# Performance work log

Hardware: AMD Instinct MI355X
Metric: run time of the kernel (lower is better)

The kernel has to match this reference:

```python
import jax, jax.numpy as jnp
import numpy as np

N_NODES = 50000
N_EDGES = 600000
F_IN = 128
HID = 128
N_CLASSES = 10


def _gcn_graph(edge_index, n_nodes):
    # PyG GCNConv: add self-loops, deg computed on target (col) with weight 1,
    # norm_e = deg^-1/2[src] * deg^-1/2[dst]
    src = jnp.concatenate([edge_index[0], jnp.arange(n_nodes, dtype=edge_index.dtype)])
    dst = jnp.concatenate([edge_index[1], jnp.arange(n_nodes, dtype=edge_index.dtype)])
    deg = jax.ops.segment_sum(jnp.ones_like(dst, dtype=jnp.float32), dst, num_segments=n_nodes)
    dinv = jnp.where(deg > 0, jax.lax.rsqrt(deg), 0.0)
    norm = dinv[src] * dinv[dst]  # [E+N]
    return src, dst, norm


def _gcn_layer(x, W, b, src, dst, norm, n_nodes):
    h = x @ W                      # [N, out] linear first (bias applied post-agg)
    m = h[src] * norm[:, None]     # gather + scale, [E+N, out]
    out = jax.ops.segment_sum(m, dst, num_segments=n_nodes)  # scatter-add
    return out + b


def setup_inputs() -> dict:
    key = jax.random.key(0)
    ks = jax.random.split(key, 4)
    x = jax.random.normal(ks[0], (N_NODES, F_IN), dtype=jnp.float32)
    edge_index = jax.random.randint(ks[1], (2, N_EDGES), 0, N_NODES, dtype=jnp.int64)
    # Glorot-ish init scale for weights
    W_stack = jax.random.normal(ks[2], (8, HID, HID), dtype=jnp.float32) * (1.0 / np.sqrt(HID))
    b_stack = jnp.zeros((8, HID), dtype=jnp.float32)
    W_out = jax.random.normal(ks[3], (HID, N_CLASSES), dtype=jnp.float32) * (1.0 / np.sqrt(HID))
    b_out = jnp.zeros((N_CLASSES,), dtype=jnp.float32)
    return {"x": x, "edge_index": edge_index, "W_stack": W_stack, "b_stack": b_stack,
            "W_out": W_out, "b_out": b_out}


def reference(x, edge_index, W_stack, b_stack, W_out, b_out):
    n_nodes = x.shape[0]
    src, dst, norm = _gcn_graph(edge_index, n_nodes)
    h = x
    for i in range(8):  # conv1..conv8 with ELU
        h = jax.nn.elu(_gcn_layer(h, W_stack[i], b_stack[i], src, dst, norm, n_nodes))
    # conv9: no activation
    return _gcn_layer(h, W_out, b_out, src, dst, norm, n_nodes)
```

## Files before the change

kernel.cpp:

```cpp
#include <hip/hip_runtime.h>
#include <math.h>

#define NN 50000
#define NE 600000
#define HID 128
#define NCLS 10
#define BK 32


__global__ __launch_bounds__(256) void k_count(const int* __restrict__ edge,
                                               int* __restrict__ counts) {
    int e = blockIdx.x * 256 + threadIdx.x;
    if (e < NE) atomicAdd(&counts[edge[NE + e]], 1);
}

__device__ __forceinline__ int wave_incl_scan(int x, int lane) {
#pragma unroll
    for (int off = 1; off < 64; off <<= 1) {
        int y = __shfl_up(x, off, 64);
        if (lane >= off) x += y;
    }
    return x;
}

__global__ __launch_bounds__(256) void k_scan1(const int* __restrict__ counts,
                                               int* __restrict__ rowptr,
                                               int* __restrict__ bsum,
                                               float* __restrict__ dinv) {
    __shared__ int ws[4];
    int tid = threadIdx.x;
    int i = blockIdx.x * 256 + tid;
    int lane = tid & 63, wv = tid >> 6;
    int v = (i < NN) ? counts[i] : 0;
    if (i < NN) dinv[i] = rsqrtf((float)(v + 1));
    int x = wave_incl_scan(v, lane);
    if (lane == 63) ws[wv] = x;
    __syncthreads();
    int off = 0;
    for (int j = 0; j < wv; ++j) off += ws[j];
    if (i < NN) rowptr[i] = off + x - v;
    if (tid == 255) bsum[blockIdx.x] = off + x;
}

__global__ __launch_bounds__(256) void k_scan2(int* __restrict__ bsum, int n) {
    __shared__ int ws[4];
    int tid = threadIdx.x;
    int lane = tid & 63, wv = tid >> 6;
    int v = (tid < n) ? bsum[tid] : 0;
    int x = wave_incl_scan(v, lane);
    if (lane == 63) ws[wv] = x;
    __syncthreads();
    int off = 0;
    for (int j = 0; j < wv; ++j) off += ws[j];
    __syncthreads();
    if (tid < n) bsum[tid] = off + x - v;
}

__global__ __launch_bounds__(256) void k_scan3(int* __restrict__ rowptr,
                                               const int* __restrict__ bsum) {
    int i = blockIdx.x * 256 + threadIdx.x;
    if (i < NN) rowptr[i] += bsum[blockIdx.x];
    if (i == 0) rowptr[NN] = NE;
}

__global__ __launch_bounds__(256) void k_fill(const int* __restrict__ edge,
                                              const int* __restrict__ rowptr,
                                              int* __restrict__ cursor,
                                              const float* __restrict__ dinv,
                                              int2* __restrict__ csr) {
    int e = blockIdx.x * 256 + threadIdx.x;
    if (e >= NE) return;
    int s = edge[e], d = edge[NE + e];
    int p = rowptr[d] + atomicAdd(&cursor[d], 1);
    csr[p] = make_int2(s, __float_as_int(dinv[s] * dinv[d]));
}


__global__ __launch_bounds__(256) void k_matmul128(const float* __restrict__ H,
                                                   const float* __restrict__ W,
                                                   float* __restrict__ T) {
    __shared__ float As[BK * 128];
    __shared__ float Bs[BK * 128];
    int tid = threadIdx.x;
    int lane = tid & 63, w = tid >> 6;
    int wr = lane >> 3, wc = lane & 7;
    int wy = w >> 1, wx = w & 1;
    int lr0 = wy * 64 + wr * 8;
    int lc0 = wx * 64 + wc * 8;
    int rowBase = blockIdx.x * 128;

    int sa_row = tid >> 1;
    int sa_k = (tid & 1) * 16;
    int sa_grow = rowBase + sa_row;
    if (sa_grow >= NN) sa_grow = NN - 1;

    float acc[8][8];
#pragma unroll
    for (int i = 0; i < 8; ++i)
#pragma unroll
        for (int j = 0; j < 8; ++j) acc[i][j] = 0.f;

    for (int k0 = 0; k0 < HID; k0 += BK) {
        const float4* hsrc = (const float4*)(H + (size_t)sa_grow * HID + k0 + sa_k);
        float4 a0 = hsrc[0], a1 = hsrc[1], a2 = hsrc[2], a3 = hsrc[3];
        const float4* wsrc = (const float4*)(W + (size_t)k0 * HID);
        float4 b0 = wsrc[tid], b1 = wsrc[tid + 256], b2 = wsrc[tid + 512], b3 = wsrc[tid + 768];
        __syncthreads();
        As[(sa_k + 0) * 128 + sa_row] = a0.x;  As[(sa_k + 1) * 128 + sa_row] = a0.y;
        As[(sa_k + 2) * 128 + sa_row] = a0.z;  As[(sa_k + 3) * 128 + sa_row] = a0.w;
        As[(sa_k + 4) * 128 + sa_row] = a1.x;  As[(sa_k + 5) * 128 + sa_row] = a1.y;
        As[(sa_k + 6) * 128 + sa_row] = a1.z;  As[(sa_k + 7) * 128 + sa_row] = a1.w;
        As[(sa_k + 8) * 128 + sa_row] = a2.x;  As[(sa_k + 9) * 128 + sa_row] = a2.y;
        As[(sa_k + 10) * 128 + sa_row] = a2.z; As[(sa_k + 11) * 128 + sa_row] = a2.w;
        As[(sa_k + 12) * 128 + sa_row] = a3.x; As[(sa_k + 13) * 128 + sa_row] = a3.y;
        As[(sa_k + 14) * 128 + sa_row] = a3.z; As[(sa_k + 15) * 128 + sa_row] = a3.w;
        ((float4*)Bs)[tid] = b0;
        ((float4*)Bs)[tid + 256] = b1;
        ((float4*)Bs)[tid + 512] = b2;
        ((float4*)Bs)[tid + 768] = b3;
        __syncthreads();
#pragma unroll
        for (int kk = 0; kk < BK; ++kk) {
            float a[8], b[8];
            ((float4*)a)[0] = *(const float4*)&As[kk * 128 + lr0];
            ((float4*)a)[1] = *(const float4*)&As[kk * 128 + lr0 + 4];
            ((float4*)b)[0] = *(const float4*)&Bs[kk * 128 + lc0];
            ((float4*)b)[1] = *(const float4*)&Bs[kk * 128 + lc0 + 4];
#pragma unroll
            for (int i = 0; i < 8; ++i)
#pragma unroll
                for (int j = 0; j < 8; ++j) acc[i][j] += a[i] * b[j];
        }
    }
#pragma unroll
    for (int i = 0; i < 8; ++i) {
        int gr = rowBase + lr0 + i;
        if (gr < NN) {
            float4 o0 = {acc[i][0], acc[i][1], acc[i][2], acc[i][3]};
            float4 o1 = {acc[i][4], acc[i][5], acc[i][6], acc[i][7]};
            float4* dst = (float4*)(T + (size_t)gr * HID + lc0);
            dst[0] = o0;
            dst[1] = o1;
        }
    }
}


__global__ __launch_bounds__(256) void k_gather_agg(const float* __restrict__ T,
                                                    float* __restrict__ Hout,
                                                    const int* __restrict__ rowptr,
                                                    const int2* __restrict__ csr,
                                                    const float* __restrict__ dinv,
                                                    const float* __restrict__ bias) {
    int lane = threadIdx.x & 63;
    int node = (blockIdx.x * 256 + threadIdx.x) >> 6;
    if (node >= NN) return;
    int slot = lane >> 4, c16 = lane & 15;

    int beg = rowptr[node], end = rowptr[node + 1];
    float4 acc0 = {0.f, 0.f, 0.f, 0.f}, acc1 = {0.f, 0.f, 0.f, 0.f};
    const int2 zed = make_int2(0, 0);

    int i = beg + slot;
    int2 e0 = (i < end) ? csr[i] : zed;
    int2 e1 = (i + 4 < end) ? csr[i + 4] : zed;
    for (; i < end; i += 8) {
        int2 p0 = (i + 8 < end) ? csr[i + 8] : zed;
        int2 p1 = (i + 12 < end) ? csr[i + 12] : zed;
        const float4* s0 = (const float4*)(T + (size_t)e0.x * HID) + c16 * 2;
        const float4* s1 = (const float4*)(T + (size_t)e1.x * HID) + c16 * 2;
        float4 u0 = s0[0], u1 = s0[1];
        float4 v0 = s1[0], v1 = s1[1];
        float w0 = __int_as_float(e0.y);
        float w1 = __int_as_float(e1.y);
        acc0.x += w0 * u0.x; acc0.y += w0 * u0.y; acc0.z += w0 * u0.z; acc0.w += w0 * u0.w;
        acc1.x += w0 * u1.x; acc1.y += w0 * u1.y; acc1.z += w0 * u1.z; acc1.w += w0 * u1.w;
        acc0.x += w1 * v0.x; acc0.y += w1 * v0.y; acc0.z += w1 * v0.z; acc0.w += w1 * v0.w;
        acc1.x += w1 * v1.x; acc1.y += w1 * v1.y; acc1.z += w1 * v1.z; acc1.w += w1 * v1.w;
        e0 = p0; e1 = p1;
    }
    acc0.x += __shfl_xor(acc0.x, 16, 64); acc0.y += __shfl_xor(acc0.y, 16, 64);
    acc0.z += __shfl_xor(acc0.z, 16, 64); acc0.w += __shfl_xor(acc0.w, 16, 64);
    acc1.x += __shfl_xor(acc1.x, 16, 64); acc1.y += __shfl_xor(acc1.y, 16, 64);
    acc1.z += __shfl_xor(acc1.z, 16, 64); acc1.w += __shfl_xor(acc1.w, 16, 64);
    acc0.x += __shfl_xor(acc0.x, 32, 64); acc0.y += __shfl_xor(acc0.y, 32, 64);
    acc0.z += __shfl_xor(acc0.z, 32, 64); acc0.w += __shfl_xor(acc0.w, 32, 64);
    acc1.x += __shfl_xor(acc1.x, 32, 64); acc1.y += __shfl_xor(acc1.y, 32, 64);
    acc1.z += __shfl_xor(acc1.z, 32, 64); acc1.w += __shfl_xor(acc1.w, 32, 64);

    if (slot == 0) {
        float sn = dinv[node];
        sn *= sn;
        const float4* trow = (const float4*)(T + (size_t)node * HID) + c16 * 2;
        float4 t0 = trow[0], t1 = trow[1];
        const float4* b4 = (const float4*)bias + c16 * 2;
        float4 b0 = b4[0], b1 = b4[1];
        float4 r0, r1;
        r0.x = acc0.x + sn * t0.x + b0.x; r0.y = acc0.y + sn * t0.y + b0.y;
        r0.z = acc0.z + sn * t0.z + b0.z; r0.w = acc0.w + sn * t0.w + b0.w;
        r1.x = acc1.x + sn * t1.x + b1.x; r1.y = acc1.y + sn * t1.y + b1.y;
        r1.z = acc1.z + sn * t1.z + b1.z; r1.w = acc1.w + sn * t1.w + b1.w;
        r0.x = r0.x > 0.f ? r0.x : expm1f(r0.x);
        r0.y = r0.y > 0.f ? r0.y : expm1f(r0.y);
        r0.z = r0.z > 0.f ? r0.z : expm1f(r0.z);
        r0.w = r0.w > 0.f ? r0.w : expm1f(r0.w);
        r1.x = r1.x > 0.f ? r1.x : expm1f(r1.x);
        r1.y = r1.y > 0.f ? r1.y : expm1f(r1.y);
        r1.z = r1.z > 0.f ? r1.z : expm1f(r1.z);
        r1.w = r1.w > 0.f ? r1.w : expm1f(r1.w);
        float4* dst = (float4*)(Hout + (size_t)node * HID) + c16 * 2;
        dst[0] = r0;
        dst[1] = r1;
    }
}


__global__ __launch_bounds__(256) void k_matmul_out(const float* __restrict__ H,
                                                    const float* __restrict__ W,
                                                    float* __restrict__ T2) {
    __shared__ float Ws[128 * 11];
    int tid = threadIdx.x;
    for (int m = tid; m < HID * NCLS; m += 256) {
        int k = m / NCLS, c = m - k * NCLS;
        Ws[k * 11 + c] = W[m];
    }
    __syncthreads();
    int row = (blockIdx.x * 256 + tid) >> 4;
    int c16 = tid & 15;
    if (row >= NN) return;
    const float* h = H + (size_t)row * HID;
    float acc[NCLS];
#pragma unroll
    for (int c = 0; c < NCLS; ++c) acc[c] = 0.f;
#pragma unroll
    for (int j = 0; j < 8; ++j) {
        float hv = h[c16 + 16 * j];
        const float* wr = &Ws[(c16 + 16 * j) * 11];
#pragma unroll
        for (int c = 0; c < NCLS; ++c) acc[c] += hv * wr[c];
    }
#pragma unroll
    for (int off = 8; off >= 1; off >>= 1) {
#pragma unroll
        for (int c = 0; c < NCLS; ++c) acc[c] += __shfl_xor(acc[c], off, 16);
    }
    if (c16 < NCLS) T2[(size_t)row * NCLS + c16] = acc[c16];
}

__global__ __launch_bounds__(256) void k_gather_out(const float* __restrict__ T2,
                                                    float* __restrict__ out,
                                                    const int* __restrict__ rowptr,
                                                    const int2* __restrict__ csr,
                                                    const float* __restrict__ dinv,
                                                    const float* __restrict__ bias) {
    int lane = threadIdx.x & 63;
    int node = (blockIdx.x * 256 + threadIdx.x) >> 6;
    if (node >= NN) return;
    int slot = lane >> 4, c = lane & 15;
    int beg = rowptr[node], end = rowptr[node + 1];
    float acc = 0.f;
    if (c < NCLS) {
        for (int i = beg + slot; i < end; i += 4) {
            int2 e = csr[i];
            acc += __int_as_float(e.y) * T2[(size_t)e.x * NCLS + c];
        }
    }
    acc += __shfl_xor(acc, 16, 64);
    acc += __shfl_xor(acc, 32, 64);
    if (slot == 0 && c < NCLS) {
        float sn = dinv[node];
        sn *= sn;
        out[node * NCLS + c] = acc + sn * T2[(size_t)node * NCLS + c] + bias[c];
    }
}


extern "C" void kernel_launch(void* const* d_in, const int* in_sizes, int n_in,
                              void* d_out, int out_size, void* d_ws, size_t ws_size,
                              hipStream_t stream) {
    (void)in_sizes; (void)n_in; (void)out_size; (void)ws_size;
    const float* x       = (const float*)d_in[0];
    const int*   edge    = (const int*)d_in[1];
    const float* W_stack = (const float*)d_in[2];
    const float* b_stack = (const float*)d_in[3];
    const float* W_out   = (const float*)d_in[4];
    const float* b_out   = (const float*)d_in[5];
    float* out = (float*)d_out;

    char* ws = (char*)d_ws;
    const size_t bigbuf = (size_t)NN * HID * sizeof(float);
    float* X      = (float*)ws;
    float* Y      = (float*)(ws + bigbuf);
    char*  p      = ws + 2 * bigbuf;
    int2*  csr    = (int2*)p;              p += sizeof(int2) * NE;
    float* dinv   = (float*)p;             p += sizeof(float) * NN;
    int*   rowptr = (int*)p;               p += sizeof(int) * (NN + 1);
    int*   counts = (int*)p;               p += sizeof(int) * NN;
    int*   bsum   = (int*)p;               p += sizeof(int) * 256;

    const int NB_N  = (NN + 255) / 256;
    const int NB_E  = (NE + 255) / 256;
    const int NB_MM = (NN + 127) / 128;
    const int NB_W  = (NN * 64 + 255) / 256;
    const int NB_O  = (NN * 16 + 255) / 256;

    hipMemsetAsync(counts, 0, sizeof(int) * NN, stream);
    k_count<<<NB_E, 256, 0, stream>>>(edge, counts);
    k_scan1<<<NB_N, 256, 0, stream>>>(counts, rowptr, bsum, dinv);
    k_scan2<<<1, 256, 0, stream>>>(bsum, NB_N);
    k_scan3<<<NB_N, 256, 0, stream>>>(rowptr, bsum);
    hipMemsetAsync(counts, 0, sizeof(int) * NN, stream);
    k_fill<<<NB_E, 256, 0, stream>>>(edge, rowptr, counts, dinv, csr);

    const float* Hin = x;
    for (int l = 0; l < 8; ++l) {
        k_matmul128<<<NB_MM, 256, 0, stream>>>(Hin, W_stack + (size_t)l * HID * HID, Y);
        k_gather_agg<<<NB_W, 256, 0, stream>>>(Y, X, rowptr, csr, dinv,
                                               b_stack + (size_t)l * HID);
        Hin = X;
    }

    k_matmul_out<<<NB_O, 256, 0, stream>>>(X, W_out, Y);
    k_gather_out<<<NB_W, 256, 0, stream>>>(Y, out, rowptr, csr, dinv, b_out);
}
```

Before: 810.1 us.

## Double-buffer matmul shared tiles and coalesce gather-agg row loads

The 128-wide matmul now uses BK=16 with two shared-memory buffers, prefetching the next K-slice into registers while computing the current one and needing only one barrier per step. Separately, the gather-aggregate kernel changes each lane's float4 access pattern from two adjacent float4s to float4s at c16 and c16+16, so the 16 lanes read contiguous 256-byte halves of a row. This is meant to hide global load latency in the GEMM and coalesce the gather. The cost is more loop iterations and more registers held for the prefetched data.

```diff
diff --git a/kernel.cpp b/kernel.cpp
--- a/kernel.cpp
+++ b/kernel.cpp
@@ -5,7 +5,7 @@
 #define NE 600000
 #define HID 128
 #define NCLS 10
-#define BK 32
+#define BK 16
 
 
 __global__ __launch_bounds__(256) void k_count(const int* __restrict__ edge,
@@ -79,8 +79,8 @@
 __global__ __launch_bounds__(256) void k_matmul128(const float* __restrict__ H,
                                                    const float* __restrict__ W,
                                                    float* __restrict__ T) {
-    __shared__ float As[BK * 128];
-    __shared__ float Bs[BK * 128];
+    __shared__ float As[2][BK * 128];
+    __shared__ float Bs[2][BK * 128];
     int tid = threadIdx.x;
     int lane = tid & 63, w = tid >> 6;
     int wr = lane >> 3, wc = lane & 7;
@@ -90,9 +90,10 @@
     int rowBase = blockIdx.x * 128;
 
     int sa_row = tid >> 1;
-    int sa_k = (tid & 1) * 16;
+    int sa_k = (tid & 1) * 8;
     int sa_grow = rowBase + sa_row;
     if (sa_grow >= NN) sa_grow = NN - 1;
+    const float* hbase = H + (size_t)sa_grow * HID + sa_k;
 
     float acc[8][8];
 #pragma unroll
@@ -100,36 +101,49 @@
 #pragma unroll
         for (int j = 0; j < 8; ++j) acc[i][j] = 0.f;
 
-    for (int k0 = 0; k0 < HID; k0 += BK) {
-        const float4* hsrc = (const float4*)(H + (size_t)sa_grow * HID + k0 + sa_k);
-        float4 a0 = hsrc[0], a1 = hsrc[1], a2 = hsrc[2], a3 = hsrc[3];
-        const float4* wsrc = (const float4*)(W + (size_t)k0 * HID);
-        float4 b0 = wsrc[tid], b1 = wsrc[tid + 256], b2 = wsrc[tid + 512], b3 = wsrc[tid + 768];
-        __syncthreads();
-        As[(sa_k + 0) * 128 + sa_row] = a0.x;  As[(sa_k + 1) * 128 + sa_row] = a0.y;
-        As[(sa_k + 2) * 128 + sa_row] = a0.z;  As[(sa_k + 3) * 128 + sa_row] = a0.w;
-        As[(sa_k + 4) * 128 + sa_row] = a1.x;  As[(sa_k + 5) * 128 + sa_row] = a1.y;
-        As[(sa_k + 6) * 128 + sa_row] = a1.z;  As[(sa_k + 7) * 128 + sa_row] = a1.w;
-        As[(sa_k + 8) * 128 + sa_row] = a2.x;  As[(sa_k + 9) * 128 + sa_row] = a2.y;
-        As[(sa_k + 10) * 128 + sa_row] = a2.z; As[(sa_k + 11) * 128 + sa_row] = a2.w;
-        As[(sa_k + 12) * 128 + sa_row] = a3.x; As[(sa_k + 13) * 128 + sa_row] = a3.y;
-        As[(sa_k + 14) * 128 + sa_row] = a3.z; As[(sa_k + 15) * 128 + sa_row] = a3.w;
-        ((float4*)Bs)[tid] = b0;
-        ((float4*)Bs)[tid + 256] = b1;
-        ((float4*)Bs)[tid + 512] = b2;
-        ((float4*)Bs)[tid + 768] = b3;
+    {
+        float4 a0 = ((const float4*)hbase)[0];
+        float4 a1 = ((const float4*)hbase)[1];
+        const float4* wsrc = (const float4*)W;
+        float4 b0 = wsrc[tid], b1 = wsrc[tid + 256];
+        As[0][(sa_k + 0) * 128 + sa_row] = a0.x; As[0][(sa_k + 1) * 128 + sa_row] = a0.y;
+        As[0][(sa_k + 2) * 128 + sa_row] = a0.z; As[0][(sa_k + 3) * 128 + sa_row] = a0.w;
+        As[0][(sa_k + 4) * 128 + sa_row] = a1.x; As[0][(sa_k + 5) * 128 + sa_row] = a1.y;
+        As[0][(sa_k + 6) * 128 + sa_row] = a1.z; As[0][(sa_k + 7) * 128 + sa_row] = a1.w;
+        ((float4*)Bs[0])[tid] = b0;
+        ((float4*)Bs[0])[tid + 256] = b1;
+    }
+
+    for (int t = 0; t < 8; ++t) {
+        int cur = t & 1;
+        float4 na0, na1, nb0, nb1;
+        if (t < 7) {
+            const float4* hn = (const float4*)(hbase + (t + 1) * BK);
+            na0 = hn[0]; na1 = hn[1];
+            const float4* wn = (const float4*)(W + (size_t)(t + 1) * BK * HID);
+            nb0 = wn[tid]; nb1 = wn[tid + 256];
+        }
         __syncthreads();
 #pragma unroll
         for (int kk = 0; kk < BK; ++kk) {
             float a[8], b[8];
-            ((float4*)a)[0] = *(const float4*)&As[kk * 128 + lr0];
-            ((float4*)a)[1] = *(const float4*)&As[kk * 128 + lr0 + 4];
-            ((float4*)b)[0] = *(const float4*)&Bs[kk * 128 + lc0];
-            ((float4*)b)[1] = *(const float4*)&Bs[kk * 128 + lc0 + 4];
+            ((float4*)a)[0] = *(const float4*)&As[cur][kk * 128 + lr0];
+            ((float4*)a)[1] = *(const float4*)&As[cur][kk * 128 + lr0 + 4];
+            ((float4*)b)[0] = *(const float4*)&Bs[cur][kk * 128 + lc0];
+            ((float4*)b)[1] = *(const float4*)&Bs[cur][kk * 128 + lc0 + 4];
 #pragma unroll
             for (int i = 0; i < 8; ++i)
 #pragma unroll
                 for (int j = 0; j < 8; ++j) acc[i][j] += a[i] * b[j];
+        }
+        if (t < 7) {
+            int nxt = 1 - cur;
+            As[nxt][(sa_k + 0) * 128 + sa_row] = na0.x; As[nxt][(sa_k + 1) * 128 + sa_row] = na0.y;
+            As[nxt][(sa_k + 2) * 128 + sa_row] = na0.z; As[nxt][(sa_k + 3) * 128 + sa_row] = na0.w;
+            As[nxt][(sa_k + 4) * 128 + sa_row] = na1.x; As[nxt][(sa_k + 5) * 128 + sa_row] = na1.y;
+            As[nxt][(sa_k + 6) * 128 + sa_row] = na1.z; As[nxt][(sa_k + 7) * 128 + sa_row] = na1.w;
+            ((float4*)Bs[nxt])[tid] = nb0;
+            ((float4*)Bs[nxt])[tid + 256] = nb1;
         }
     }
 #pragma unroll
@@ -167,10 +181,10 @@
     for (; i < end; i += 8) {
         int2 p0 = (i + 8 < end) ? csr[i + 8] : zed;
         int2 p1 = (i + 12 < end) ? csr[i + 12] : zed;
-        const float4* s0 = (const float4*)(T + (size_t)e0.x * HID) + c16 * 2;
-        const float4* s1 = (const float4*)(T + (size_t)e1.x * HID) + c16 * 2;
-        float4 u0 = s0[0], u1 = s0[1];
-        float4 v0 = s1[0], v1 = s1[1];
+        const float4* s0 = (const float4*)(T + (size_t)e0.x * HID);
+        const float4* s1 = (const float4*)(T + (size_t)e1.x * HID);
+        float4 u0 = s0[c16], u1 = s0[c16 + 16];
+        float4 v0 = s1[c16], v1 = s1[c16 + 16];
         float w0 = __int_as_float(e0.y);
         float w1 = __int_as_float(e1.y);
         acc0.x += w0 * u0.x; acc0.y += w0 * u0.y; acc0.z += w0 * u0.z; acc0.w += w0 * u0.w;
@@ -191,10 +205,10 @@
     if (slot == 0) {
         float sn = dinv[node];
         sn *= sn;
-        const float4* trow = (const float4*)(T + (size_t)node * HID) + c16 * 2;
-        float4 t0 = trow[0], t1 = trow[1];
-        const float4* b4 = (const float4*)bias + c16 * 2;
-        float4 b0 = b4[0], b1 = b4[1];
+        const float4* trow = (const float4*)(T + (size_t)node * HID);
+        float4 t0 = trow[c16], t1 = trow[c16 + 16];
+        const float4* b4 = (const float4*)bias;
+        float4 b0 = b4[c16], b1 = b4[c16 + 16];
         float4 r0, r1;
         r0.x = acc0.x + sn * t0.x + b0.x; r0.y = acc0.y + sn * t0.y + b0.y;
         r0.z = acc0.z + sn * t0.z + b0.z; r0.w = acc0.w + sn * t0.w + b0.w;
@@ -208,9 +222,9 @@
         r1.y = r1.y > 0.f ? r1.y : expm1f(r1.y);
         r1.z = r1.z > 0.f ? r1.z : expm1f(r1.z);
         r1.w = r1.w > 0.f ? r1.w : expm1f(r1.w);
-        float4* dst = (float4*)(Hout + (size_t)node * HID) + c16 * 2;
-        dst[0] = r0;
-        dst[1] = r1;
+        float4* dst = (float4*)(Hout + (size_t)node * HID);
+        dst[c16] = r0;
+        dst[c16 + 16] = r1;
     }
 }
 
```

New measurement: 912.6 us. 1.13x slower.

## Fuse whole GCN pipeline into one cooperative persistent kernel with grid syncs

Applied to the files above, without the earlier changes.

Replaces the sequence of roughly 25 kernel launches with a single cooperative persistent kernel that runs CSR construction, all matmul and gather layers, and the output layer as phases separated by grid-wide syncs. It also overlaps the first-layer matmul with the graph-building phase and changes the gather lane mapping so the 16 lanes in a slot read contiguous float4 elements. The aim is to remove per-launch overhead and idle gaps between small kernels. In exchange, grid syncs cost time, persistent blocks loop over fixed tiles with possible load imbalance, and launch_bounds(256,4) may limit registers for the 8x8 matmul accumulators.

```diff
diff --git a/kernel.cpp b/kernel.cpp
--- a/kernel.cpp
+++ b/kernel.cpp
@@ -1,18 +1,19 @@
 #include <hip/hip_runtime.h>
+#include <hip/hip_cooperative_groups.h>
 #include <math.h>
+
+namespace cg = cooperative_groups;
 
 #define NN 50000
 #define NE 600000
 #define HID 128
 #define NCLS 10
-#define BK 32
-
-
-__global__ __launch_bounds__(256) void k_count(const int* __restrict__ edge,
-                                               int* __restrict__ counts) {
-    int e = blockIdx.x * 256 + threadIdx.x;
-    if (e < NE) atomicAdd(&counts[edge[NE + e]], 1);
-}
+#define MMBK 32
+#define NTILE 391
+#define NCHUNK 196
+#define NGRP4 12500
+#define NGRP16 3125
+
 
 __device__ __forceinline__ int wave_incl_scan(int x, int lane) {
 #pragma unroll
@@ -23,71 +24,16 @@
     return x;
 }
 
-__global__ __launch_bounds__(256) void k_scan1(const int* __restrict__ counts,
-                                               int* __restrict__ rowptr,
-                                               int* __restrict__ bsum,
-                                               float* __restrict__ dinv) {
-    __shared__ int ws[4];
-    int tid = threadIdx.x;
-    int i = blockIdx.x * 256 + tid;
-    int lane = tid & 63, wv = tid >> 6;
-    int v = (i < NN) ? counts[i] : 0;
-    if (i < NN) dinv[i] = rsqrtf((float)(v + 1));
-    int x = wave_incl_scan(v, lane);
-    if (lane == 63) ws[wv] = x;
-    __syncthreads();
-    int off = 0;
-    for (int j = 0; j < wv; ++j) off += ws[j];
-    if (i < NN) rowptr[i] = off + x - v;
-    if (tid == 255) bsum[blockIdx.x] = off + x;
-}
-
-__global__ __launch_bounds__(256) void k_scan2(int* __restrict__ bsum, int n) {
-    __shared__ int ws[4];
-    int tid = threadIdx.x;
-    int lane = tid & 63, wv = tid >> 6;
-    int v = (tid < n) ? bsum[tid] : 0;
-    int x = wave_incl_scan(v, lane);
-    if (lane == 63) ws[wv] = x;
-    __syncthreads();
-    int off = 0;
-    for (int j = 0; j < wv; ++j) off += ws[j];
-    __syncthreads();
-    if (tid < n) bsum[tid] = off + x - v;
-}
-
-__global__ __launch_bounds__(256) void k_scan3(int* __restrict__ rowptr,
-                                               const int* __restrict__ bsum) {
-    int i = blockIdx.x * 256 + threadIdx.x;
-    if (i < NN) rowptr[i] += bsum[blockIdx.x];
-    if (i == 0) rowptr[NN] = NE;
-}
-
-__global__ __launch_bounds__(256) void k_fill(const int* __restrict__ edge,
-                                              const int* __restrict__ rowptr,
-                                              int* __restrict__ cursor,
-                                              const float* __restrict__ dinv,
-                                              int2* __restrict__ csr) {
-    int e = blockIdx.x * 256 + threadIdx.x;
-    if (e >= NE) return;
-    int s = edge[e], d = edge[NE + e];
-    int p = rowptr[d] + atomicAdd(&cursor[d], 1);
-    csr[p] = make_int2(s, __float_as_int(dinv[s] * dinv[d]));
-}
-
-
-__global__ __launch_bounds__(256) void k_matmul128(const float* __restrict__ H,
-                                                   const float* __restrict__ W,
-                                                   float* __restrict__ T) {
-    __shared__ float As[BK * 128];
-    __shared__ float Bs[BK * 128];
-    int tid = threadIdx.x;
+__device__ __forceinline__ void dev_matmul_tile(const float* __restrict__ H,
+                                                const float* __restrict__ W,
+                                                float* __restrict__ T,
+                                                int rowBase, int tid,
+                                                float* As, float* Bs) {
     int lane = tid & 63, w = tid >> 6;
     int wr = lane >> 3, wc = lane & 7;
     int wy = w >> 1, wx = w & 1;
     int lr0 = wy * 64 + wr * 8;
     int lc0 = wx * 64 + wc * 8;
-    int rowBase = blockIdx.x * 128;
 
     int sa_row = tid >> 1;
     int sa_k = (tid & 1) * 16;
@@ -100,7 +46,7 @@
 #pragma unroll
         for (int j = 0; j < 8; ++j) acc[i][j] = 0.f;
 
-    for (int k0 = 0; k0 < HID; k0 += BK) {
+    for (int k0 = 0; k0 < HID; k0 += MMBK) {
         const float4* hsrc = (const float4*)(H + (size_t)sa_grow * HID + k0 + sa_k);
         float4 a0 = hsrc[0], a1 = hsrc[1], a2 = hsrc[2], a3 = hsrc[3];
         const float4* wsrc = (const float4*)(W + (size_t)k0 * HID);
@@ -120,7 +66,7 @@
         ((float4*)Bs)[tid + 768] = b3;
         __syncthreads();
 #pragma unroll
-        for (int kk = 0; kk < BK; ++kk) {
+        for (int kk = 0; kk < MMBK; ++kk) {
             float a[8], b[8];
             ((float4*)a)[0] = *(const float4*)&As[kk * 128 + lr0];
             ((float4*)a)[1] = *(const float4*)&As[kk * 128 + lr0 + 4];
@@ -145,18 +91,14 @@
     }
 }
 
-
-__global__ __launch_bounds__(256) void k_gather_agg(const float* __restrict__ T,
-                                                    float* __restrict__ Hout,
-                                                    const int* __restrict__ rowptr,
-                                                    const int2* __restrict__ csr,
-                                                    const float* __restrict__ dinv,
-                                                    const float* __restrict__ bias) {
-    int lane = threadIdx.x & 63;
-    int node = (blockIdx.x * 256 + threadIdx.x) >> 6;
-    if (node >= NN) return;
+__device__ __forceinline__ void dev_gather_node(const float* __restrict__ T,
+                                                float* __restrict__ Hout,
+                                                const int* __restrict__ rowptr,
+                                                const int2* __restrict__ csr,
+                                                const float* __restrict__ dinv,
+                                                const float* __restrict__ bias,
+                                                int node, int lane) {
     int slot = lane >> 4, c16 = lane & 15;
-
     int beg = rowptr[node], end = rowptr[node + 1];
     float4 acc0 = {0.f, 0.f, 0.f, 0.f}, acc1 = {0.f, 0.f, 0.f, 0.f};
     const int2 zed = make_int2(0, 0);
@@ -167,10 +109,10 @@
     for (; i < end; i += 8) {
         int2 p0 = (i + 8 < end) ? csr[i + 8] : zed;
         int2 p1 = (i + 12 < end) ? csr[i + 12] : zed;
-        const float4* s0 = (const float4*)(T + (size_t)e0.x * HID) + c16 * 2;
-        const float4* s1 = (const float4*)(T + (size_t)e1.x * HID) + c16 * 2;
-        float4 u0 = s0[0], u1 = s0[1];
-        float4 v0 = s1[0], v1 = s1[1];
+        const float4* s0 = (const float4*)(T + (size_t)e0.x * HID);
+        const float4* s1 = (const float4*)(T + (size_t)e1.x * HID);
+        float4 u0 = s0[c16], u1 = s0[c16 + 16];
+        float4 v0 = s1[c16], v1 = s1[c16 + 16];
         float w0 = __int_as_float(e0.y);
         float w1 = __int_as_float(e1.y);
         acc0.x += w0 * u0.x; acc0.y += w0 * u0.y; acc0.z += w0 * u0.z; acc0.w += w0 * u0.w;
@@ -191,10 +133,10 @@
     if (slot == 0) {
         float sn = dinv[node];
         sn *= sn;
-        const float4* trow = (const float4*)(T + (size_t)node * HID) + c16 * 2;
-        float4 t0 = trow[0], t1 = trow[1];
-        const float4* b4 = (const float4*)bias + c16 * 2;
-        float4 b0 = b4[0], b1 = b4[1];
+        const float4* trow = (const float4*)(T + (size_t)node * HID);
+        float4 t0 = trow[c16], t1 = trow[c16 + 16];
+        const float4* b4 = (const float4*)bias;
+        float4 b0 = b4[c16], b1 = b4[c16 + 16];
         float4 r0, r1;
         r0.x = acc0.x + sn * t0.x + b0.x; r0.y = acc0.y + sn * t0.y + b0.y;
         r0.z = acc0.z + sn * t0.z + b0.z; r0.w = acc0.w + sn * t0.w + b0.w;
@@ -208,12 +150,239 @@
         r1.y = r1.y > 0.f ? r1.y : expm1f(r1.y);
         r1.z = r1.z > 0.f ? r1.z : expm1f(r1.z);
         r1.w = r1.w > 0.f ? r1.w : expm1f(r1.w);
-        float4* dst = (float4*)(Hout + (size_t)node * HID) + c16 * 2;
-        dst[0] = r0;
-        dst[1] = r1;
-    }
-}
-
+        float4* dst = (float4*)(Hout + (size_t)node * HID);
+        dst[c16] = r0;
+        dst[c16 + 16] = r1;
+    }
+}
+
+__device__ __forceinline__ void dev_outmat_row(const float* __restrict__ H,
+                                               const float* __restrict__ Ws,
+                                               float* __restrict__ T2,
+                                               int row, int c16) {
+    const float* h = H + (size_t)row * HID;
+    float acc[NCLS];
+#pragma unroll
+    for (int c = 0; c < NCLS; ++c) acc[c] = 0.f;
+#pragma unroll
+    for (int j = 0; j < 8; ++j) {
+        float hv = h[c16 + 16 * j];
+        const float* wr = &Ws[(c16 + 16 * j) * 11];
+#pragma unroll
+        for (int c = 0; c < NCLS; ++c) acc[c] += hv * wr[c];
+    }
+#pragma unroll
+    for (int off = 8; off >= 1; off >>= 1) {
+#pragma unroll
+        for (int c = 0; c < NCLS; ++c) acc[c] += __shfl_xor(acc[c], off, 16);
+    }
+    if (c16 < NCLS) T2[(size_t)row * NCLS + c16] = acc[c16];
+}
+
+__device__ __forceinline__ void dev_outgather_node(const float* __restrict__ T2,
+                                                   float* __restrict__ out,
+                                                   const int* __restrict__ rowptr,
+                                                   const int2* __restrict__ csr,
+                                                   const float* __restrict__ dinv,
+                                                   const float* __restrict__ bias,
+                                                   int node, int lane) {
+    int slot = lane >> 4, c = lane & 15;
+    int beg = rowptr[node], end = rowptr[node + 1];
+    float acc = 0.f;
+    if (c < NCLS) {
+        for (int i = beg + slot; i < end; i += 4) {
+            int2 e = csr[i];
+            acc += __int_as_float(e.y) * T2[(size_t)e.x * NCLS + c];
+        }
+    }
+    acc += __shfl_xor(acc, 16, 64);
+    acc += __shfl_xor(acc, 32, 64);
+    if (slot == 0 && c < NCLS) {
+        float sn = dinv[node];
+        sn *= sn;
+        out[node * NCLS + c] = acc + sn * T2[(size_t)node * NCLS + c] + bias[c];
+    }
+}
+
+
+__global__ __launch_bounds__(256, 4) void k_mega(const float* __restrict__ x,
+                                                 const int* __restrict__ edge,
+                                                 const float* __restrict__ W_stack,
+                                                 const float* __restrict__ b_stack,
+                                                 const float* __restrict__ W_out,
+                                                 const float* __restrict__ b_out,
+                                                 float* __restrict__ out,
+                                                 float* __restrict__ X,
+                                                 float* __restrict__ Y,
+                                                 int2* __restrict__ csr,
+                                                 float* __restrict__ dinv,
+                                                 int* __restrict__ rowptr,
+                                                 int* __restrict__ counts,
+                                                 int* __restrict__ bsum) {
+    cg::grid_group gg = cg::this_grid();
+    __shared__ float smem[8192];
+    float* As = smem;
+    float* Bs = smem + MMBK * 128;
+    int tid = threadIdx.x, bid = blockIdx.x;
+    int gsz = gridDim.x * 256, gtid = bid * 256 + tid;
+
+    for (int i = gtid; i < NN; i += gsz) counts[i] = 0;
+    for (int t = bid; t < NTILE; t += gridDim.x)
+        dev_matmul_tile(x, W_stack, Y, t * 128, tid, As, Bs);
+    gg.sync();
+    for (int e = gtid; e < NE; e += gsz) atomicAdd(&counts[edge[NE + e]], 1);
+    gg.sync();
+    {
+        int* ws = (int*)smem;
+        for (int c = bid; c < NCHUNK; c += gridDim.x) {
+            int i = c * 256 + tid;
+            int lane = tid & 63, wv = tid >> 6;
+            int v = (i < NN) ? counts[i] : 0;
+            if (i < NN) dinv[i] = rsqrtf((float)(v + 1));
+            int xs = wave_incl_scan(v, lane);
+            __syncthreads();
+            if (lane == 63) ws[wv] = xs;
+            __syncthreads();
+            int off = 0;
+            for (int j = 0; j < wv; ++j) off += ws[j];
+            if (i < NN) rowptr[i] = off + xs - v;
+            if (tid == 255) bsum[c] = off + xs;
+        }
+    }
+    gg.sync();
+    if (bid == 0) {
+        int* ws = (int*)smem;
+        int lane = tid & 63, wv = tid >> 6;
+        int v = (tid < NCHUNK) ? bsum[tid] : 0;
+        int xs = wave_incl_scan(v, lane);
+        if (lane == 63) ws[wv] = xs;
+        __syncthreads();
+        int off = 0;
+        for (int j = 0; j < wv; ++j) off += ws[j];
+        if (tid < NCHUNK) bsum[tid] = off + xs - v;
+    }
+    gg.sync();
+    for (int i = gtid; i < NN; i += gsz) {
+        rowptr[i] += bsum[i >> 8];
+        counts[i] = 0;
+    }
+    if (gtid == 0) rowptr[NN] = NE;
+    gg.sync();
+    for (int e = gtid; e < NE; e += gsz) {
+        int s = edge[e], d = edge[NE + e];
+        int pq = rowptr[d] + atomicAdd(&counts[d], 1);
+        csr[pq] = make_int2(s, __float_as_int(dinv[s] * dinv[d]));
+    }
+    gg.sync();
+    for (int l = 1; l < 8; ++l) {
+        const float* bias = b_stack + (size_t)(l - 1) * HID;
+        for (int g = bid; g < NGRP4; g += gridDim.x)
+            dev_gather_node(Y, X, rowptr, csr, dinv, bias, g * 4 + (tid >> 6), tid & 63);
+        gg.sync();
+        for (int t = bid; t < NTILE; t += gridDim.x)
+            dev_matmul_tile(X, W_stack + (size_t)l * HID * HID, Y, t * 128, tid, As, Bs);
+        gg.sync();
+    }
+    for (int g = bid; g < NGRP4; g += gridDim.x)
+        dev_gather_node(Y, X, rowptr, csr, dinv, b_stack + 7 * HID, g * 4 + (tid >> 6), tid & 63);
+    gg.sync();
+    {
+        float* Ws = smem;
+        for (int m = tid; m < HID * NCLS; m += 256) {
+            int k = m / NCLS, c = m - k * NCLS;
+            Ws[k * 11 + c] = W_out[m];
+        }
+        __syncthreads();
+        for (int g = bid; g < NGRP16; g += gridDim.x)
+            dev_outmat_row(X, Ws, Y, g * 16 + (tid >> 4), tid & 15);
+    }
+    gg.sync();
+    for (int g = bid; g < NGRP4; g += gridDim.x)
+        dev_outgather_node(Y, out, rowptr, csr, dinv, b_out, g * 4 + (tid >> 6), tid & 63);
+}
+
+
+__global__ __launch_bounds__(256) void k_count(const int* __restrict__ edge,
+                                               int* __restrict__ counts) {
+    int e = blockIdx.x * 256 + threadIdx.x;
+    if (e < NE) atomicAdd(&counts[edge[NE + e]], 1);
+}
+
+__global__ __launch_bounds__(256) void k_zero(int* __restrict__ p, int n) {
+    int i = blockIdx.x * 256 + threadIdx.x;
+    if (i < n) p[i] = 0;
+}
+
+__global__ __launch_bounds__(256) void k_scan1(const int* __restrict__ counts,
+                                               int* __restrict__ rowptr,
+                                               int* __restrict__ bsum,
+                                               float* __restrict__ dinv) {
+    __shared__ int ws[4];
+    int tid = threadIdx.x;
+    int i = blockIdx.x * 256 + tid;
+    int lane = tid & 63, wv = tid >> 6;
+    int v = (i < NN) ? counts[i] : 0;
+    if (i < NN) dinv[i] = rsqrtf((float)(v + 1));
+    int x = wave_incl_scan(v, lane);
+    if (lane == 63) ws[wv] = x;
+    __syncthreads();
+    int off = 0;
+    for (int j = 0; j < wv; ++j) off += ws[j];
+    if (i < NN) rowptr[i] = off + x - v;
+    if (tid == 255) bsum[blockIdx.x] = off + x;
+}
+
+__global__ __launch_bounds__(256) void k_scan2(int* __restrict__ bsum, int n) {
+    __shared__ int ws[4];
+    int tid = threadIdx.x;
+    int lane = tid & 63, wv = tid >> 6;
+    int v = (tid < n) ? bsum[tid] : 0;
+    int x = wave_incl_scan(v, lane);
+    if (lane == 63) ws[wv] = x;
+    __syncthreads();
+    int off = 0;
+    for (int j = 0; j < wv; ++j) off += ws[j];
+    __syncthreads();
+    if (tid < n) bsum[tid] = off + x - v;
+}
+
+__global__ __launch_bounds__(256) void k_scan3(int* __restrict__ rowptr,
+                                               const int* __restrict__ bsum) {
+    int i = blockIdx.x * 256 + threadIdx.x;
+    if (i < NN) rowptr[i] += bsum[blockIdx.x];
+    if (i == 0) rowptr[NN] = NE;
+}
+
+__global__ __launch_bounds__(256) void k_fill(const int* __restrict__ edge,
+                                              const int* __restrict__ rowptr,
+                                              int* __restrict__ cursor,
+                                              const float* __restrict__ dinv,
+                                              int2* __restrict__ csr) {
+    int e = blockIdx.x * 256 + threadIdx.x;
+    if (e >= NE) return;
+    int s = edge[e], d = edge[NE + e];
+    int p = rowptr[d] + atomicAdd(&cursor[d], 1);
+    csr[p] = make_int2(s, __float_as_int(dinv[s] * dinv[d]));
+}
+
+__global__ __launch_bounds__(256) void k_matmul128(const float* __restrict__ H,
+                                                   const float* __restrict__ W,
+                                                   float* __restrict__ T) {
+    __shared__ float As[MMBK * 128];
+    __shared__ float Bs[MMBK * 128];
+    dev_matmul_tile(H, W, T, blockIdx.x * 128, threadIdx.x, As, Bs);
+}
+
+__global__ __launch_bounds__(256) void k_gather_agg(const float* __restrict__ T,
+                                                    float* __restrict__ Hout,
+                                                    const int* __restrict__ rowptr,
+                                                    const int2* __restrict__ csr,
+                                                    const float* __restrict__ dinv,
+                                                    const float* __restrict__ bias) {
+    int node = (blockIdx.x * 256 + threadIdx.x) >> 6;
+    if (node >= NN) return;
+    dev_gather_node(T, Hout, rowptr, csr, dinv, bias, node, threadIdx.x & 63);
+}
 
 __global__ __launch_bounds__(256) void k_matmul_out(const float* __restrict__ H,
                                                     const float* __restrict__ W,
@@ -226,25 +395,8 @@
     }
     __syncthreads();
     int row = (blockIdx.x * 256 + tid) >> 4;
-    int c16 = tid & 15;
     if (row >= NN) return;
-    const float* h = H + (size_t)row * HID;
-    float acc[NCLS];
-#pragma unroll
-    for (int c = 0; c < NCLS; ++c) acc[c] = 0.f;
-#pragma unroll
-    for (int j = 0; j < 8; ++j) {
-        float hv = h[c16 + 16 * j];
-        const float* wr = &Ws[(c16 + 16 * j) * 11];
-#pragma unroll
-        for (int c = 0; c < NCLS; ++c) acc[c] += hv * wr[c];
-    }
-#pragma unroll
-    for (int off = 8; off >= 1; off >>= 1) {
-#pragma unroll
-        for (int c = 0; c < NCLS; ++c) acc[c] += __shfl_xor(acc[c], off, 16);
-    }
-    if (c16 < NCLS) T2[(size_t)row * NCLS + c16] = acc[c16];
+    dev_outmat_row(H, Ws, T2, row, tid & 15);
 }
 
 __global__ __launch_bounds__(256) void k_gather_out(const float* __restrict__ T2,
@@ -253,25 +405,9 @@
                                                     const int2* __restrict__ csr,
                                                     const float* __restrict__ dinv,
                                                     const float* __restrict__ bias) {
-    int lane = threadIdx.x & 63;
     int node = (blockIdx.x * 256 + threadIdx.x) >> 6;
     if (node >= NN) return;
-    int slot = lane >> 4, c = lane & 15;
-    int beg = rowptr[node], end = rowptr[node + 1];
-    float acc = 0.f;
-    if (c < NCLS) {
-        for (int i = beg + slot; i < end; i += 4) {
-            int2 e = csr[i];
-            acc += __int_as_float(e.y) * T2[(size_t)e.x * NCLS + c];
-        }
-    }
-    acc += __shfl_xor(acc, 16, 64);
-    acc += __shfl_xor(acc, 32, 64);
-    if (slot == 0 && c < NCLS) {
-        float sn = dinv[node];
-        sn *= sn;
-        out[node * NCLS + c] = acc + sn * T2[(size_t)node * NCLS + c] + bias[c];
-    }
+    dev_outgather_node(T2, out, rowptr, csr, dinv, bias, node, threadIdx.x & 63);
 }
 
 
@@ -298,18 +434,32 @@
     int*   counts = (int*)p;               p += sizeof(int) * NN;
     int*   bsum   = (int*)p;               p += sizeof(int) * 256;
 
+    int maxB = 0;
+    hipError_t qerr = hipOccupancyMaxActiveBlocksPerMultiprocessor(&maxB, k_mega, 256, 0);
+    if (qerr == hipSuccess && maxB >= 1) {
+        int grid = maxB * 256;
+        if (grid > 2048) grid = 2048;
+        void* args[] = {(void*)&x,       (void*)&edge,  (void*)&W_stack, (void*)&b_stack,
+                        (void*)&W_out,   (void*)&b_out, (void*)&out,     (void*)&X,
+                        (void*)&Y,       (void*)&csr,   (void*)&dinv,    (void*)&rowptr,
+                        (void*)&counts,  (void*)&bsum};
+        hipError_t lerr = hipLaunchCooperativeKernel((const void*)k_mega, dim3(grid),
+                                                     dim3(256), args, 0, stream);
+        if (lerr == hipSuccess) return;
+    }
+
     const int NB_N  = (NN + 255) / 256;
     const int NB_E  = (NE + 255) / 256;
-    const int NB_MM = (NN + 127) / 128;
+    const int NB_MM = NTILE;
     const int NB_W  = (NN * 64 + 255) / 256;
     const int NB_O  = (NN * 16 + 255) / 256;
 
-    hipMemsetAsync(counts, 0, sizeof(int) * NN, stream);
+    k_zero<<<NB_N, 256, 0, stream>>>(counts, NN);
     k_count<<<NB_E, 256, 0, stream>>>(edge, counts);
     k_scan1<<<NB_N, 256, 0, stream>>>(counts, rowptr, bsum, dinv);
     k_scan2<<<1, 256, 0, stream>>>(bsum, NB_N);
     k_scan3<<<NB_N, 256, 0, stream>>>(rowptr, bsum);
-    hipMemsetAsync(counts, 0, sizeof(int) * NN, stream);
+    k_zero<<<NB_N, 256, 0, stream>>>(counts, NN);
     k_fill<<<NB_E, 256, 0, stream>>>(edge, rowptr, counts, dinv, csr);
 
     const float* Hin = x;
@@ -319,7 +469,6 @@
                                                b_stack + (size_t)l * HID);
         Hin = X;
     }
-
     k_matmul_out<<<NB_O, 256, 0, stream>>>(X, W_out, Y);
     k_gather_out<<<NB_W, 256, 0, stream>>>(Y, out, rowptr, csr, dinv, b_out);
 }
```

Measured after the change: 2.751 ms. 240% more time.

## Split gather-aggregate into column slices across blocks, replace memsets with kernels

Applied to the files above, without the earlier changes.

Replaces the per-node full-row gather with a kernel in which each block handles one 16-column slice for 16 nodes. Blocks are interleaved by slice so that neighbouring blocks hit different column ranges of the same rows, probably to improve cache locality. Each lane gathers float4 from 16 edges in parallel and reduces with shuffles. It drops the software prefetch of CSR entries and reads the CSR once per slice, 8 times in total. hipMemsetAsync calls are also replaced by a small zeroing kernel to cut API overhead.

```diff
diff --git a/kernel.cpp b/kernel.cpp
--- a/kernel.cpp
+++ b/kernel.cpp
@@ -7,6 +7,11 @@
 #define NCLS 10
 #define BK 32
 
+
+__global__ __launch_bounds__(256) void k_zero(int* __restrict__ p, int n) {
+    int i = blockIdx.x * 256 + threadIdx.x;
+    if (i < n) p[i] = 0;
+}
 
 __global__ __launch_bounds__(256) void k_count(const int* __restrict__ edge,
                                                int* __restrict__ counts) {
@@ -146,71 +151,54 @@
 }
 
 
-__global__ __launch_bounds__(256) void k_gather_agg(const float* __restrict__ T,
-                                                    float* __restrict__ Hout,
-                                                    const int* __restrict__ rowptr,
-                                                    const int2* __restrict__ csr,
-                                                    const float* __restrict__ dinv,
-                                                    const float* __restrict__ bias) {
-    int lane = threadIdx.x & 63;
-    int node = (blockIdx.x * 256 + threadIdx.x) >> 6;
-    if (node >= NN) return;
-    int slot = lane >> 4, c16 = lane & 15;
-
-    int beg = rowptr[node], end = rowptr[node + 1];
-    float4 acc0 = {0.f, 0.f, 0.f, 0.f}, acc1 = {0.f, 0.f, 0.f, 0.f};
-    const int2 zed = make_int2(0, 0);
-
-    int i = beg + slot;
-    int2 e0 = (i < end) ? csr[i] : zed;
-    int2 e1 = (i + 4 < end) ? csr[i + 4] : zed;
-    for (; i < end; i += 8) {
-        int2 p0 = (i + 8 < end) ? csr[i + 8] : zed;
-        int2 p1 = (i + 12 < end) ? csr[i + 12] : zed;
-        const float4* s0 = (const float4*)(T + (size_t)e0.x * HID) + c16 * 2;
-        const float4* s1 = (const float4*)(T + (size_t)e1.x * HID) + c16 * 2;
-        float4 u0 = s0[0], u1 = s0[1];
-        float4 v0 = s1[0], v1 = s1[1];
-        float w0 = __int_as_float(e0.y);
-        float w1 = __int_as_float(e1.y);
-        acc0.x += w0 * u0.x; acc0.y += w0 * u0.y; acc0.z += w0 * u0.z; acc0.w += w0 * u0.w;
-        acc1.x += w0 * u1.x; acc1.y += w0 * u1.y; acc1.z += w0 * u1.z; acc1.w += w0 * u1.w;
-        acc0.x += w1 * v0.x; acc0.y += w1 * v0.y; acc0.z += w1 * v0.z; acc0.w += w1 * v0.w;
-        acc1.x += w1 * v1.x; acc1.y += w1 * v1.y; acc1.z += w1 * v1.z; acc1.w += w1 * v1.w;
-        e0 = p0; e1 = p1;
-    }
-    acc0.x += __shfl_xor(acc0.x, 16, 64); acc0.y += __shfl_xor(acc0.y, 16, 64);
-    acc0.z += __shfl_xor(acc0.z, 16, 64); acc0.w += __shfl_xor(acc0.w, 16, 64);
-    acc1.x += __shfl_xor(acc1.x, 16, 64); acc1.y += __shfl_xor(acc1.y, 16, 64);
-    acc1.z += __shfl_xor(acc1.z, 16, 64); acc1.w += __shfl_xor(acc1.w, 16, 64);
-    acc0.x += __shfl_xor(acc0.x, 32, 64); acc0.y += __shfl_xor(acc0.y, 32, 64);
-    acc0.z += __shfl_xor(acc0.z, 32, 64); acc0.w += __shfl_xor(acc0.w, 32, 64);
-    acc1.x += __shfl_xor(acc1.x, 32, 64); acc1.y += __shfl_xor(acc1.y, 32, 64);
-    acc1.z += __shfl_xor(acc1.z, 32, 64); acc1.w += __shfl_xor(acc1.w, 32, 64);
-
-    if (slot == 0) {
-        float sn = dinv[node];
-        sn *= sn;
-        const float4* trow = (const float4*)(T + (size_t)node * HID) + c16 * 2;
-        float4 t0 = trow[0], t1 = trow[1];
-        const float4* b4 = (const float4*)bias + c16 * 2;
-        float4 b0 = b4[0], b1 = b4[1];
-        float4 r0, r1;
-        r0.x = acc0.x + sn * t0.x + b0.x; r0.y = acc0.y + sn * t0.y + b0.y;
-        r0.z = acc0.z + sn * t0.z + b0.z; r0.w = acc0.w + sn * t0.w + b0.w;
-        r1.x = acc1.x + sn * t1.x + b1.x; r1.y = acc1.y + sn * t1.y + b1.y;
-        r1.z = acc1.z + sn * t1.z + b1.z; r1.w = acc1.w + sn * t1.w + b1.w;
-        r0.x = r0.x > 0.f ? r0.x : expm1f(r0.x);
-        r0.y = r0.y > 0.f ? r0.y : expm1f(r0.y);
-        r0.z = r0.z > 0.f ? r0.z : expm1f(r0.z);
-        r0.w = r0.w > 0.f ? r0.w : expm1f(r0.w);
-        r1.x = r1.x > 0.f ? r1.x : expm1f(r1.x);
-        r1.y = r1.y > 0.f ? r1.y : expm1f(r1.y);
-        r1.z = r1.z > 0.f ? r1.z : expm1f(r1.z);
-        r1.w = r1.w > 0.f ? r1.w : expm1f(r1.w);
-        float4* dst = (float4*)(Hout + (size_t)node * HID) + c16 * 2;
-        dst[0] = r0;
-        dst[1] = r1;
+__global__ __launch_bounds__(256) void k_gather_slice(const float* __restrict__ T,
+                                                      float* __restrict__ Hout,
+                                                      const int* __restrict__ rowptr,
+                                                      const int2* __restrict__ csr,
+                                                      const float* __restrict__ dinv,
+                                                      const float* __restrict__ bias) {
+    int bid = blockIdx.x;
+    int slice = bid & 7;
+    int nblk = bid >> 3;
+    int wv = threadIdx.x >> 6, lane = threadIdx.x & 63;
+    int slot = lane >> 2;
+    int l4 = lane & 3;
+    int col0 = slice * 16 + l4 * 4;
+    float4 bb = *(const float4*)(bias + col0);
+
+#pragma unroll
+    for (int n = 0; n < 4; ++n) {
+        int node = nblk * 16 + wv * 4 + n;
+        int beg = rowptr[node], end = rowptr[node + 1];
+        float4 acc = {0.f, 0.f, 0.f, 0.f};
+        for (int i = beg + slot; i < end; i += 16) {
+            int2 e = csr[i];
+            float w = __int_as_float(e.y);
+            float4 v = *(const float4*)(T + (size_t)e.x * HID + col0);
+            acc.x += w * v.x; acc.y += w * v.y; acc.z += w * v.z; acc.w += w * v.w;
+        }
+#pragma unroll
+        for (int off = 4; off < 64; off <<= 1) {
+            acc.x += __shfl_xor(acc.x, off, 64);
+            acc.y += __shfl_xor(acc.y, off, 64);
+            acc.z += __shfl_xor(acc.z, off, 64);
+            acc.w += __shfl_xor(acc.w, off, 64);
+        }
+        if (slot == 0) {
+            float sn = dinv[node];
+            sn *= sn;
+            float4 t = *(const float4*)(T + (size_t)node * HID + col0);
+            float4 r;
+            r.x = acc.x + sn * t.x + bb.x;
+            r.y = acc.y + sn * t.y + bb.y;
+            r.z = acc.z + sn * t.z + bb.z;
+            r.w = acc.w + sn * t.w + bb.w;
+            r.x = r.x > 0.f ? r.x : expm1f(r.x);
+            r.y = r.y > 0.f ? r.y : expm1f(r.y);
+            r.z = r.z > 0.f ? r.z : expm1f(r.z);
+            r.w = r.w > 0.f ? r.w : expm1f(r.w);
+            *(float4*)(Hout + (size_t)node * HID + col0) = r;
+        }
     }
 }
 
@@ -301,22 +289,23 @@
     const int NB_N  = (NN + 255) / 256;
     const int NB_E  = (NE + 255) / 256;
     const int NB_MM = (NN + 127) / 128;
+    const int NB_G  = 8 * (NN / 16);
     const int NB_W  = (NN * 64 + 255) / 256;
     const int NB_O  = (NN * 16 + 255) / 256;
 
-    hipMemsetAsync(counts, 0, sizeof(int) * NN, stream);
+    k_zero<<<NB_N, 256, 0, stream>>>(counts, NN);
     k_count<<<NB_E, 256, 0, stream>>>(edge, counts);
     k_scan1<<<NB_N, 256, 0, stream>>>(counts, rowptr, bsum, dinv);
     k_scan2<<<1, 256, 0, stream>>>(bsum, NB_N);
     k_scan3<<<NB_N, 256, 0, stream>>>(rowptr, bsum);
-    hipMemsetAsync(counts, 0, sizeof(int) * NN, stream);
+    k_zero<<<NB_N, 256, 0, stream>>>(counts, NN);
     k_fill<<<NB_E, 256, 0, stream>>>(edge, rowptr, counts, dinv, csr);
 
     const float* Hin = x;
     for (int l = 0; l < 8; ++l) {
         k_matmul128<<<NB_MM, 256, 0, stream>>>(Hin, W_stack + (size_t)l * HID * HID, Y);
-        k_gather_agg<<<NB_W, 256, 0, stream>>>(Y, X, rowptr, csr, dinv,
-                                               b_stack + (size_t)l * HID);
+        k_gather_slice<<<NB_G, 256, 0, stream>>>(Y, X, rowptr, csr, dinv,
+                                                 b_stack + (size_t)l * HID);
         Hin = X;
     }
 
```

After: 1.276 ms. 57.5% more time.
